# Kernel optimization log

Hardware: AMD Instinct MI355X
Metric: run time of the kernel (lower is better)

The kernel has to match this reference:

```python
import jax, jax.numpy as jnp
import numpy as np
from functools import partial


def edt_sq(mask):
    """Exact squared Euclidean distance transform (distance from True pixels to
    nearest False pixel), separable two-pass algorithm. mask: bool (..., H, W).
    Matches scipy.ndimage.distance_transform_edt(mask)**2 whenever each 2-D
    slice contains at least one background (False) pixel."""
    H, W = mask.shape[-2], mask.shape[-1]
    LARGE = jnp.float32(H * H + W * W + 1)

    # ---- pass 1: 1-D distance to nearest False along H (rows axis) ----
    mm = jnp.moveaxis(mask, -2, 0)  # (H, ..., W)
    init = jnp.full(mm.shape[1:], LARGE, dtype=jnp.float32)

    def step1(carry, x):
        d = jnp.where(x, carry + 1.0, 0.0)
        return d, d

    _, fwd = jax.lax.scan(step1, init, mm)
    _, bwd = jax.lax.scan(step1, init, mm[::-1])
    d1 = jnp.minimum(fwd, bwd[::-1])            # (H, ..., W) 1-D distance
    f = jnp.minimum(d1 * d1, LARGE)             # squared, capped
    f = jnp.moveaxis(f, 0, -2)                  # (..., H, W)

    # ---- pass 2: D[..., j] = min_k f[..., k] + (j - k)^2 along W ----
    j = jnp.arange(W, dtype=jnp.float32)
    fT = jnp.moveaxis(f, -1, 0)                 # (W, ..., H)

    def step2(D, xk):
        fk, k = xk                               # fk: (..., H)
        cand = fk[..., None] + (j - k) ** 2      # (..., H, W)
        return jnp.minimum(D, cand), None

    D0 = jnp.full(f.shape, LARGE, dtype=jnp.float32)
    D, _ = jax.lax.scan(step2, D0, (fT, j))
    return D


def setup_inputs() -> dict:
    key = jax.random.key(0)
    k1, k2 = jax.random.split(key)
    output = jax.random.normal(k1, (16, 2, 512, 512), dtype=jnp.float32)
    target = jax.random.randint(k2, (16, 512, 512), 0, 2).astype(jnp.int64)
    return {"output": output, "target": target}


def reference(output, target):
    B, C, H, W = output.shape
    probs = jax.nn.softmax(output, axis=1)                    # (B,C,H,W)
    y_onehot = jax.nn.one_hot(target, C, axis=1, dtype=jnp.float32)

    # distance maps only needed for channels 1: (loop starts at c=1)
    pc_mask = probs[:, 1:] > 0.5                              # (B,C-1,H,W)
    gt_mask = y_onehot[:, 1:] > 0.5
    pc_dist_sq = edt_sq(pc_mask)
    gt_dist_sq = edt_sq(gt_mask)
    dist = jax.lax.stop_gradient(pc_dist_sq + gt_dist_sq)     # no_grad in torch

    pred_error = (probs - y_onehot) ** 2                      # (B,C,H,W)
    multipled = pred_error[:, 1:] * dist                      # einsum 'bcxy,bcxy->bcxy'
    return multipled.mean()
```

## Files before the change

### kernel.cpp

```cpp
#include <hip/hip_runtime.h>

#define BB   16
#define HH   512
#define WW   512
#define HWSZ (HH * WW)
#define NPIX (BB * HWSZ)
#define LARGE_F 524289.0f
#define NW 16
#define GR 4
#define NLOSSBLK (BB * HH / GR)


__global__ __launch_bounds__(512) void pack_kernel(
    const float* __restrict__ out4,
    const int* __restrict__ target,
    unsigned int* __restrict__ bitsG) {
  __shared__ unsigned char mbyte[32 * 256];

  const int w    = blockIdx.x >> 1;
  const int half = blockIdx.x & 1;
  const int b    = blockIdx.y;
  const int c0   = half * 256;
  const float* ch0 = out4 + (size_t)(b * 2) * HWSZ;
  const float* ch1 = ch0 + HWSZ;
  const int* tb = target + (size_t)b * HWSZ;

#pragma unroll
  for (int s = 0; s < 4; ++s) {
    int q  = s * 512 + threadIdx.x;
    int i  = q >> 6;
    int cq = (q & 63) * 4;
    int g  = (w * 32 + i) * WW + c0 + cq;
    float4 a0 = *(const float4*)(ch0 + g);
    float4 a1 = *(const float4*)(ch1 + g);
    int4   t4 = *(const int4*)(tb + g);
    unsigned p = 0;
    p |= (unsigned)(((a1.x > a0.x) ? 1u : 0u) | ((t4.x == 1) ? 2u : 0u));
    p |= (unsigned)(((a1.y > a0.y) ? 1u : 0u) | ((t4.y == 1) ? 2u : 0u)) << 8;
    p |= (unsigned)(((a1.z > a0.z) ? 1u : 0u) | ((t4.z == 1) ? 2u : 0u)) << 16;
    p |= (unsigned)(((a1.w > a0.w) ? 1u : 0u) | ((t4.w == 1) ? 2u : 0u)) << 24;
    *(unsigned*)&mbyte[i * 256 + cq] = p;
  }
  __syncthreads();

  {
    int c   = threadIdx.x & 255;
    int sel = threadIdx.x >> 8;
    unsigned wd = 0;
#pragma unroll
    for (int k = 0; k < 32; ++k) {
      unsigned mb = mbyte[k * 256 + c];
      wd |= ((mb >> sel) & 1u) << k;
    }
    bitsG[(size_t)((b * 2 + sel) * NW + w) * WW + c0 + c] = wd;
  }
}

__device__ __forceinline__ int colprobe(const unsigned (*lb)[WW],
                                        const unsigned* __restrict__ gcol,
                                        int wlo, int whi, int j, int i) {
  int w = i >> 5, bp = i & 31;
  unsigned cur = lb[w - wlo][j];
  unsigned zu = ~cur & (0xFFFFFFFFu >> (31 - bp));
  unsigned zd = ~cur & (0xFFFFFFFFu << bp);
  int up = 0xFFFF, dn = 0xFFFF;
  if (zu) {
    up = bp - (31 - __clz(zu));
  } else {
    for (int ww = w - 1; ww >= 0; --ww) {
      unsigned z = ~((ww >= wlo) ? lb[ww - wlo][j] : gcol[ww * WW]);
      if (z) { up = i - (ww * 32 + 31 - __clz(z)); break; }
    }
  }
  if (zd) {
    dn = (__ffs((int)zd) - 1) - bp;
  } else {
    for (int ww = w + 1; ww < NW; ++ww) {
      unsigned z = ~((ww <= whi) ? lb[ww - wlo][j] : gcol[ww * WW]);
      if (z) { dn = ww * 32 + (__ffs((int)z) - 1) - i; break; }
    }
  }
  return min(min(up, dn), 0xFFFF);
}

__global__ __launch_bounds__(512) void loss_kernel(
    const float* __restrict__ out4,
    const unsigned int* __restrict__ bitsG,
    float* __restrict__ partials) {
  __shared__ unsigned lbits[2][5][WW];
  __shared__ float2 fv[GR][WW];
  __shared__ float ssum[8];

  const int b  = blockIdx.x >> 7;
  const int i0 = (blockIdx.x & 127) * GR;
  const int j  = threadIdx.x;

  const int wc  = i0 >> 5;
  const int wlo = max(0, wc - 2);
  const int whi = min(NW - 1, wc + 2);
  const int nwr = whi - wlo + 1;

  const unsigned* gb = bitsG + (size_t)(b * 2) * NW * WW;
  for (int idx = threadIdx.x; idx < nwr * 2 * WW; idx += 512) {
    int c    = idx & (WW - 1);
    int rest = idx >> 9;
    int wrel = rest >> 1;
    int sel  = rest & 1;
    lbits[sel][wrel][c] = gb[(size_t)(sel * NW + wlo + wrel) * WW + c];
  }

  const float* xp = out4 + (size_t)(b * 2) * HWSZ + (size_t)i0 * WW;
  float x0v[GR], x1v[GR];
#pragma unroll
  for (int rw = 0; rw < GR; ++rw) {
    x0v[rw] = xp[rw * WW + j];
    x1v[rw] = xp[HWSZ + rw * WW + j];
  }
  __syncthreads();

  const unsigned* gpc = gb + j;
  const unsigned* ggt = gb + NW * WW + j;
  float y1v[GR];
  float bpc[GR], bgt[GR];
#pragma unroll
  for (int rw = 0; rw < GR; ++rw) {
    int i = i0 + rw;
    int rpc = colprobe(lbits[0], gpc, wlo, whi, j, i);
    int rgt = colprobe(lbits[1], ggt, wlo, whi, j, i);
    float fpc = (rpc >= 512) ? LARGE_F : (float)(rpc * rpc);
    float fgt = (rgt >= 512) ? LARGE_F : (float)(rgt * rgt);
    fv[rw][j] = make_float2(fpc, fgt);
    bpc[rw] = fpc; bgt[rw] = fgt;
    y1v[rw] = (rgt != 0) ? 1.0f : 0.0f;
  }
  __syncthreads();

  for (int r = 1; r < WW; ++r) {
    float rr = (float)(r * r);
    float mx = fmaxf(fmaxf(fmaxf(bpc[0], bgt[0]), fmaxf(bpc[1], bgt[1])),
                     fmaxf(fmaxf(bpc[2], bgt[2]), fmaxf(bpc[3], bgt[3])));
    if (rr >= mx) break;
    int jl = j - r, jr = j + r;
    if (jl >= 0) {
#pragma unroll
      for (int rw = 0; rw < GR; ++rw) {
        float2 a = fv[rw][jl];
        bpc[rw] = fminf(bpc[rw], a.x + rr);
        bgt[rw] = fminf(bgt[rw], a.y + rr);
      }
    }
    if (jr < WW) {
#pragma unroll
      for (int rw = 0; rw < GR; ++rw) {
        float2 a = fv[rw][jr];
        bpc[rw] = fminf(bpc[rw], a.x + rr);
        bgt[rw] = fminf(bgt[rw], a.y + rr);
      }
    }
  }

  float contrib = 0.0f;
#pragma unroll
  for (int rw = 0; rw < GR; ++rw) {
    float p1 = 1.0f / (1.0f + expf(x0v[rw] - x1v[rw]));
    float d = p1 - y1v[rw];
    contrib += d * d * (bpc[rw] + bgt[rw]);
  }
  contrib *= (1.0f / (float)NPIX);

  for (int off = 32; off > 0; off >>= 1) contrib += __shfl_down(contrib, off);
  int lane = threadIdx.x & 63;
  int wave = threadIdx.x >> 6;
  if (lane == 0) ssum[wave] = contrib;
  __syncthreads();
  if (threadIdx.x == 0) {
    float s = 0.0f;
#pragma unroll
    for (int w = 0; w < 8; ++w) s += ssum[w];
    partials[blockIdx.x] = s;
  }
}

__global__ __launch_bounds__(1024) void reduce_kernel(
    const float* __restrict__ partials, float* __restrict__ d_out) {
  __shared__ float ssum[16];
  float s = 0.0f;
#pragma unroll
  for (int k = 0; k < NLOSSBLK / 1024; ++k)
    s += partials[k * 1024 + threadIdx.x];
  for (int off = 32; off > 0; off >>= 1) s += __shfl_down(s, off);
  int lane = threadIdx.x & 63;
  int wave = threadIdx.x >> 6;
  if (lane == 0) ssum[wave] = s;
  __syncthreads();
  if (threadIdx.x == 0) {
    float t = 0.0f;
#pragma unroll
    for (int w = 0; w < 16; ++w) t += ssum[w];
    *d_out = t;
  }
}

extern "C" void kernel_launch(void* const* d_in, const int* in_sizes, int n_in,
                              void* d_out, int out_size, void* d_ws, size_t ws_size,
                              hipStream_t stream) {
  const float* out4 = (const float*)d_in[0];
  const int* target = (const int*)d_in[1];
  unsigned int* bitsG = (unsigned int*)d_ws;
  float* partials = (float*)(bitsG + BB * 2 * NW * WW);
  float* out = (float*)d_out;

  dim3 grid1(32, BB);
  pack_kernel<<<grid1, 512, 0, stream>>>(out4, target, bitsG);

  loss_kernel<<<NLOSSBLK, 512, 0, stream>>>(out4, bitsG, partials);

  reduce_kernel<<<1, 1024, 0, stream>>>(partials, out);
}
```

Measured before the change: 103.7 us.

## Precompute squared prediction error in pack kernel and double rows per loss block

Measured after the change: 104.7 us. No clear change (+1.0%).

```diff
diff --git a/kernel.cpp b/kernel.cpp
--- a/kernel.cpp
+++ b/kernel.cpp
@@ -7,14 +7,15 @@
 #define NPIX (BB * HWSZ)
 #define LARGE_F 524289.0f
 #define NW 16
-#define GR 4
+#define GR 8
 #define NLOSSBLK (BB * HH / GR)
 
 
 __global__ __launch_bounds__(512) void pack_kernel(
     const float* __restrict__ out4,
     const int* __restrict__ target,
-    unsigned int* __restrict__ bitsG) {
+    unsigned int* __restrict__ bitsG,
+    float* __restrict__ eG) {
   __shared__ unsigned char mbyte[32 * 256];
 
   const int w    = blockIdx.x >> 1;
@@ -24,6 +25,7 @@
   const float* ch0 = out4 + (size_t)(b * 2) * HWSZ;
   const float* ch1 = ch0 + HWSZ;
   const int* tb = target + (size_t)b * HWSZ;
+  float* eb = eG + (size_t)b * HWSZ;
 
 #pragma unroll
   for (int s = 0; s < 4; ++s) {
@@ -40,6 +42,29 @@
     p |= (unsigned)(((a1.z > a0.z) ? 1u : 0u) | ((t4.z == 1) ? 2u : 0u)) << 16;
     p |= (unsigned)(((a1.w > a0.w) ? 1u : 0u) | ((t4.w == 1) ? 2u : 0u)) << 24;
     *(unsigned*)&mbyte[i * 256 + cq] = p;
+
+    float4 e4;
+    {
+      float p1 = 1.0f / (1.0f + expf(a0.x - a1.x));
+      float d  = p1 - ((t4.x == 1) ? 1.0f : 0.0f);
+      e4.x = d * d;
+    }
+    {
+      float p1 = 1.0f / (1.0f + expf(a0.y - a1.y));
+      float d  = p1 - ((t4.y == 1) ? 1.0f : 0.0f);
+      e4.y = d * d;
+    }
+    {
+      float p1 = 1.0f / (1.0f + expf(a0.z - a1.z));
+      float d  = p1 - ((t4.z == 1) ? 1.0f : 0.0f);
+      e4.z = d * d;
+    }
+    {
+      float p1 = 1.0f / (1.0f + expf(a0.w - a1.w));
+      float d  = p1 - ((t4.w == 1) ? 1.0f : 0.0f);
+      e4.w = d * d;
+    }
+    *(float4*)(eb + g) = e4;
   }
   __syncthreads();
 
@@ -84,15 +109,15 @@
 }
 
 __global__ __launch_bounds__(512) void loss_kernel(
-    const float* __restrict__ out4,
+    const float* __restrict__ eG,
     const unsigned int* __restrict__ bitsG,
     float* __restrict__ partials) {
   __shared__ unsigned lbits[2][5][WW];
   __shared__ float2 fv[GR][WW];
   __shared__ float ssum[8];
 
-  const int b  = blockIdx.x >> 7;
-  const int i0 = (blockIdx.x & 127) * GR;
+  const int b  = blockIdx.x >> 6;
+  const int i0 = (blockIdx.x & 63) * GR;
   const int j  = threadIdx.x;
 
   const int wc  = i0 >> 5;
@@ -109,18 +134,14 @@
     lbits[sel][wrel][c] = gb[(size_t)(sel * NW + wlo + wrel) * WW + c];
   }
 
-  const float* xp = out4 + (size_t)(b * 2) * HWSZ + (size_t)i0 * WW;
-  float x0v[GR], x1v[GR];
-#pragma unroll
-  for (int rw = 0; rw < GR; ++rw) {
-    x0v[rw] = xp[rw * WW + j];
-    x1v[rw] = xp[HWSZ + rw * WW + j];
-  }
+  const float* ep = eG + (size_t)b * HWSZ + (size_t)i0 * WW;
+  float ev[GR];
+#pragma unroll
+  for (int rw = 0; rw < GR; ++rw) ev[rw] = ep[rw * WW + j];
   __syncthreads();
 
   const unsigned* gpc = gb + j;
   const unsigned* ggt = gb + NW * WW + j;
-  float y1v[GR];
   float bpc[GR], bgt[GR];
 #pragma unroll
   for (int rw = 0; rw < GR; ++rw) {
@@ -131,14 +152,14 @@
     float fgt = (rgt >= 512) ? LARGE_F : (float)(rgt * rgt);
     fv[rw][j] = make_float2(fpc, fgt);
     bpc[rw] = fpc; bgt[rw] = fgt;
-    y1v[rw] = (rgt != 0) ? 1.0f : 0.0f;
   }
   __syncthreads();
 
   for (int r = 1; r < WW; ++r) {
     float rr = (float)(r * r);
-    float mx = fmaxf(fmaxf(fmaxf(bpc[0], bgt[0]), fmaxf(bpc[1], bgt[1])),
-                     fmaxf(fmaxf(bpc[2], bgt[2]), fmaxf(bpc[3], bgt[3])));
+    float mx = 0.0f;
+#pragma unroll
+    for (int rw = 0; rw < GR; ++rw) mx = fmaxf(mx, fmaxf(bpc[rw], bgt[rw]));
     if (rr >= mx) break;
     int jl = j - r, jr = j + r;
     if (jl >= 0) {
@@ -161,11 +182,7 @@
 
   float contrib = 0.0f;
 #pragma unroll
-  for (int rw = 0; rw < GR; ++rw) {
-    float p1 = 1.0f / (1.0f + expf(x0v[rw] - x1v[rw]));
-    float d = p1 - y1v[rw];
-    contrib += d * d * (bpc[rw] + bgt[rw]);
-  }
+  for (int rw = 0; rw < GR; ++rw) contrib += ev[rw] * (bpc[rw] + bgt[rw]);
   contrib *= (1.0f / (float)NPIX);
 
   for (int off = 32; off > 0; off >>= 1) contrib += __shfl_down(contrib, off);
@@ -184,10 +201,7 @@
 __global__ __launch_bounds__(1024) void reduce_kernel(
     const float* __restrict__ partials, float* __restrict__ d_out) {
   __shared__ float ssum[16];
-  float s = 0.0f;
-#pragma unroll
-  for (int k = 0; k < NLOSSBLK / 1024; ++k)
-    s += partials[k * 1024 + threadIdx.x];
+  float s = partials[threadIdx.x];
   for (int off = 32; off > 0; off >>= 1) s += __shfl_down(s, off);
   int lane = threadIdx.x & 63;
   int wave = threadIdx.x >> 6;
@@ -207,13 +221,14 @@
   const float* out4 = (const float*)d_in[0];
   const int* target = (const int*)d_in[1];
   unsigned int* bitsG = (unsigned int*)d_ws;
-  float* partials = (float*)(bitsG + BB * 2 * NW * WW);
+  float* eG = (float*)(bitsG + BB * 2 * NW * WW);
+  float* partials = eG + NPIX;
   float* out = (float*)d_out;
 
   dim3 grid1(32, BB);
-  pack_kernel<<<grid1, 512, 0, stream>>>(out4, target, bitsG);
-
-  loss_kernel<<<NLOSSBLK, 512, 0, stream>>>(out4, bitsG, partials);
+  pack_kernel<<<grid1, 512, 0, stream>>>(out4, target, bitsG, eG);
+
+  loss_kernel<<<NLOSSBLK, 512, 0, stream>>>(eG, bitsG, partials);
 
   reduce_kernel<<<1, 1024, 0, stream>>>(partials, out);
 }
```
